# Performance work log

Measured on AMD Instinct MI355X. Metric: run time of the kernel, lower is better.

The kernel has to match this reference:

```python
import jax, jax.numpy as jnp
import numpy as np
from math import factorial

# ---------- Clebsch-Gordan coefficients for real spherical harmonics (e3nn convention) ----------

def _su2_cg(j1, j2, j3, m1, m2, m3):
    if m3 != m1 + m2:
        return 0.0
    f = factorial
    vmin = max(-j1 + j2 + m3, -j1 + m1, 0)
    vmax = min(j2 + j3 + m1, j3 - j1 + j2, j3 + m3)
    C = ((2 * j3 + 1)
         * f(j3 + j1 - j2) * f(j3 - j1 + j2) * f(j1 + j2 - j3) / f(j1 + j2 + j3 + 1)
         * f(j3 + m3) * f(j3 - m3)
         / (f(j1 - m1) * f(j1 + m1) * f(j2 - m2) * f(j2 + m2))) ** 0.5
    S = 0.0
    for v in range(vmin, vmax + 1):
        S += ((-1) ** (v + j2 + m2) / f(v)
              * f(j2 + j3 + m1 - v) * f(j1 - m1 + v)
              / f(j3 - j1 + j2 - v) / f(j3 + m3 - v) / f(v + j1 - j2 - m3))
    return C * S

def _q(l):  # change of basis real -> complex SH
    q = np.zeros((2 * l + 1, 2 * l + 1), dtype=np.complex128)
    for m in range(-l, 0):
        q[l + m, l + abs(m)] = 2 ** -0.5
        q[l + m, l - abs(m)] = -1j * 2 ** -0.5
    q[l, l] = 1.0
    for m in range(1, l + 1):
        q[l + m, l + abs(m)] = (-1) ** m * 2 ** -0.5
        q[l + m, l - abs(m)] = 1j * (-1) ** m * 2 ** -0.5
    return (-1j) ** l * q

def _real_cg(l1, l2, l3):
    Cc = np.zeros((2 * l1 + 1, 2 * l2 + 1, 2 * l3 + 1), dtype=np.complex128)
    for i, m1 in enumerate(range(-l1, l1 + 1)):
        for j, m2 in enumerate(range(-l2, l2 + 1)):
            for k, m3 in enumerate(range(-l3, l3 + 1)):
                Cc[i, j, k] = _su2_cg(l1, l2, l3, m1, m2, m3)
    Cr = np.einsum('ij,kl,nm,ikn->jlm', _q(l1), _q(l2), np.conj(_q(l3)), Cc)
    assert np.abs(Cr.imag).max() < 1e-8
    return np.real(Cr)

def _build_K(l1max, l2max, l3max):
    d1, d2, d3 = (l1max + 1) ** 2, (l2max + 1) ** 2, (l3max + 1) ** 2
    K = np.zeros((d1, d2, d3), dtype=np.float32)
    for l1 in range(l1max + 1):
        for l2 in range(l2max + 1):
            for l3 in range(abs(l1 - l2), min(l3max, l1 + l2) + 1):
                K[l1 * l1:(l1 + 1) ** 2, l2 * l2:(l2 + 1) ** 2, l3 * l3:(l3 + 1) ** 2] += _real_cg(l1, l2, l3)
    return K

_K1 = jnp.asarray(_build_K(1, 2, 3))   # [4, 9, 16]
_K2 = jnp.asarray(_build_K(3, 2, 5))   # [16, 9, 36]
_L2MAX_DIM = 9

def _real_sh_l2(d):
    # orthonormal real SH up to l=2 for unit vectors d [E,3] -> [E,9], m = -l..l
    x, y, z = d[:, 0], d[:, 1], d[:, 2]
    c0 = 0.28209479177387814
    c1 = 0.4886025119029199
    c2a = 1.0925484305920792
    c2b = 0.31539156525252005
    c2c = 0.5462742152960396
    return jnp.stack([
        jnp.full_like(x, c0),
        c1 * y, c1 * z, c1 * x,
        c2a * x * y, c2a * y * z, c2b * (3.0 * z * z - 1.0), c2a * x * z, c2c * (x * x - y * y),
    ], axis=-1)


def setup_inputs() -> dict:
    key = jax.random.key(0)
    ks = jax.random.split(key, 9)
    N, E, G, C = 51200, 819200, 64, 10
    return {
        'positions': jax.random.normal(ks[0], (N, 3), jnp.float32),
        'w1': jax.random.normal(ks[1], (1, 1), jnp.float32) * 0.5,
        'b1': jax.random.normal(ks[2], (1,), jnp.float32) * 0.1,
        'w2': jax.random.normal(ks[3], (1, 1), jnp.float32) * 0.5,
        'b2': jax.random.normal(ks[4], (1,), jnp.float32) * 0.1,
        'wg': jax.random.normal(ks[5], (72, C), jnp.float32) * 0.1,
        'bg': jax.random.normal(ks[6], (C,), jnp.float32) * 0.1,
        'senders': jax.random.randint(ks[7], (E,), 0, N, dtype=jnp.int32),
        'receivers': jax.random.randint(ks[8], (E,), 0, N, dtype=jnp.int32),
        'n_graphs': G,
    }


def reference(positions, w1, b1, w2, b2, wg, bg, senders, receivers, n_graphs):
    N = positions.shape[0]
    E = senders.shape[0]
    # edge direction spherical harmonics (normalize=True)
    d = positions[receivers] - positions[senders]
    d = d / (jnp.linalg.norm(d, axis=-1, keepdims=True) + 1e-12)
    Y = _real_sh_l2(d)                                   # [E, 9]
    # route SH degrees into parity channels: even parity (l=0,2) -> ch 0, odd (l=1) -> ch 1
    sh = jnp.zeros((E, 2, _L2MAX_DIM), Y.dtype)
    sh = sh.at[:, 0, 0].set(Y[:, 0])
    sh = sh.at[:, 1, 1:4].set(Y[:, 1:4])
    sh = sh.at[:, 0, 4:9].set(Y[:, 4:9])
    sh_flip = sh[:, ::-1]                                # parity-swapped view

    def layer(x, K, w, b, denom):
        xs = x[senders]                                  # [E, 2, d1, f]
        # per-edge equivariant tensor product; p3=0 pairs same parities, p3=1 opposite
        t0 = jnp.einsum('ijk,epif,epj->ekf', K, xs, sh)
        t1 = jnp.einsum('ijk,epif,epj->ekf', K, xs, sh_flip)
        tp = jnp.stack([t0, t1], axis=1)                 # [E, 2, d3, f]
        agg = jax.ops.segment_sum(tp, receivers, num_segments=N) / denom
        return jnp.einsum('npkf,fg->npkg', agg, w) + b   # Dense over feature dim

    x = jnp.ones((N, 2, 4, 1), Y.dtype)                  # graphs._replace(nodes=ones)
    x = layer(x, _K1, w1, b1, 1.0)                       # [N, 2, 16, 1]
    x = layer(x, _K2, w2, b2, 1.0)                       # [N, 2, 36, 1]

    # global readout: segment-sum nodes per graph, flatten, Dense -> num_classes
    gidx = jnp.repeat(jnp.arange(n_graphs), N // n_graphs)
    g = jax.ops.segment_sum(x, gidx, num_segments=n_graphs)  # [G, 2, 36, 1]
    logits = g.reshape(n_graphs, -1) @ wg + bg               # [G, 10]
    return logits
```

## Files before the change

kernel.cpp:

```cpp
#include <hip/hip_runtime.h>

__device__ __constant__ double FACT[12] = {
    1.0, 1.0, 2.0, 6.0, 24.0, 120.0, 720.0, 5040.0,
    40320.0, 362880.0, 3628800.0, 39916800.0
};

struct cplx { double re, im; };
__device__ __forceinline__ cplx cmul(cplx a, cplx b) {
    return { a.re * b.re - a.im * b.im, a.re * b.im + a.im * b.re };
}

__device__ double su2_cg_full(int j1, int j2, int j3, int m1, int m2, int m3) {
    if (j3 < abs(j1 - j2) || j3 > j1 + j2) return 0.0;
    if (abs(m1) > j1 || abs(m2) > j2 || abs(m3) > j3) return 0.0;
    if (m3 != m1 + m2) return 0.0;
    int vmin = max(max(-j1 + j2 + m3, -j1 + m1), 0);
    int vmax = min(min(j2 + j3 + m1, j3 - j1 + j2), j3 + m3);
    if (vmax < vmin) return 0.0;
    double C = sqrt((2.0 * j3 + 1.0) * FACT[j3 + j1 - j2] * FACT[j3 - j1 + j2] *
                    FACT[j1 + j2 - j3] / FACT[j1 + j2 + j3 + 1] *
                    FACT[j3 + m3] * FACT[j3 - m3] /
                    (FACT[j1 - m1] * FACT[j1 + m1] * FACT[j2 - m2] * FACT[j2 + m2]));
    double S = 0.0;
    for (int v = vmin; v <= vmax; ++v) {
        double sgn = ((v + j2 + m2) & 1) ? -1.0 : 1.0;
        S += sgn / FACT[v] * FACT[j2 + j3 + m1 - v] * FACT[j1 - m1 + v] /
             FACT[j3 - j1 + j2 - v] / FACT[j3 + m3 - v] / FACT[v + j1 - j2 - m3];
    }
    return C * S;
}

__device__ __forceinline__ int su2_idx(int l1, int l2, int l3, int m1, int m2, int m3) {
    return ((((l1 * 3 + l2) * 6 + l3) * 7 + (m1 + 3)) * 5 + (m2 + 2)) * 11 + (m3 + 5);
}
#define SU2_TAB_SIZE 27720

__device__ int q_col(int l, int c0, int* rows, cplx* vals) {
    const double s = 0.7071067811865476;
    cplx ph;
    switch (l & 3) {
        case 0: ph = {1.0, 0.0}; break;
        case 1: ph = {0.0, -1.0}; break;
        case 2: ph = {-1.0, 0.0}; break;
        default: ph = {0.0, 1.0}; break;
    }
    int mu = c0 - l;
    if (mu == 0) { rows[0] = l; vals[0] = ph; return 1; }
    if (mu > 0) {
        rows[0] = l - mu; vals[0] = cmul(ph, {s, 0.0});
        double sg = (mu & 1) ? -1.0 : 1.0;
        rows[1] = l + mu; vals[1] = cmul(ph, {sg * s, 0.0});
        return 2;
    }
    int am = -mu;
    rows[0] = l - am; vals[0] = cmul(ph, {0.0, -s});
    double sg = (am & 1) ? -1.0 : 1.0;
    rows[1] = l + am; vals[1] = cmul(ph, {0.0, sg * s});
    return 2;
}

__device__ float real_cg_elem_tab(const double* __restrict__ su2tab,
                                  int l1, int l2, int l3, int a, int b, int c) {
    int r1[2], r2[2], r3[2];
    cplx v1[2], v2[2], v3[2];
    int n1 = q_col(l1, a, r1, v1);
    int n2 = q_col(l2, b, r2, v2);
    int n3 = q_col(l3, c, r3, v3);
    double re = 0.0;
    for (int x = 0; x < n1; ++x)
        for (int y = 0; y < n2; ++y)
            for (int z = 0; z < n3; ++z) {
                cplx qq = cmul(v1[x], v2[y]);
                cplx q3c = { v3[z].re, -v3[z].im };
                qq = cmul(qq, q3c);
                double cg = su2tab[su2_idx(l1, l2, l3, r1[x] - l1, r2[y] - l2, r3[z] - l3)];
                re += qq.re * cg;
            }
    return (float)re;
}

__device__ int flsqrt(int x) {
    int l = 0;
    while ((l + 1) * (l + 1) <= x) ++l;
    return l;
}

__device__ __forceinline__ void sh_from_delta(float dx, float dy, float dz, float* Y) {
    float inv = 1.f / (sqrtf(dx * dx + dy * dy + dz * dz) + 1e-12f);
    float x = dx * inv, y = dy * inv, z = dz * inv;
    const float c1 = 0.4886025119029199f;
    const float c2a = 1.0925484305920792f;
    Y[0] = 0.28209479177387814f;
    Y[1] = c1 * y; Y[2] = c1 * z; Y[3] = c1 * x;
    Y[4] = c2a * x * y;
    Y[5] = c2a * y * z;
    Y[6] = 0.31539156525252005f * (3.f * z * z - 1.f);
    Y[7] = c2a * x * z;
    Y[8] = 0.5462742152960396f * (x * x - y * y);
}

__device__ void tbl2_work(const double* __restrict__ su2tab, int t,
                          float* __restrict__ A1, float* __restrict__ K2) {
    const int NK2 = 16 * 9 * 36;
    if (t < NK2) {
        int k = t % 36;
        int j = (t / 36) % 9;
        int i = t / (36 * 9);
        int l1 = flsqrt(i), l2 = flsqrt(j), l3 = flsqrt(k);
        float v = 0.f;
        if (l3 >= abs(l1 - l2) && l3 <= l1 + l2)
            v = real_cg_elem_tab(su2tab, l1, l2, l3, i - l1 * l1, j - l2 * l2, k - l3 * l3);
        K2[t] = v;
    } else if (t < NK2 + 144) {
        int u = t - NK2;
        int j = u / 16, k = u % 16;
        int l2 = flsqrt(j), l3 = flsqrt(k);
        float v = 0.f;
        for (int i = 0; i < 4; ++i) {
            int l1 = flsqrt(i);
            if (l3 >= abs(l1 - l2) && l3 <= l1 + l2 && l3 <= 3)
                v += real_cg_elem_tab(su2tab, l1, l2, l3, i - l1 * l1, j - l2 * l2, k - l3 * l3);
        }
        A1[u] = v;
    }
}

#define SU2_BLOCKS 109
__global__ __launch_bounds__(256) void phase1_k(double* __restrict__ su2tab,
                                                float* __restrict__ zero_base,
                                                long zeroN) {
    if (blockIdx.x < SU2_BLOCKS) {
        int t = blockIdx.x * 256 + threadIdx.x;
        if (t < SU2_TAB_SIZE) {
            int r = t;
            int im3 = r % 11; r /= 11;
            int im2 = r % 5;  r /= 5;
            int im1 = r % 7;  r /= 7;
            int l3  = r % 6;  r /= 6;
            int l2  = r % 3;  r /= 3;
            int l1  = r;
            su2tab[t] = su2_cg_full(l1, l2, l3, im1 - 3, im2 - 2, im3 - 5);
        }
    } else {
        long zb = blockIdx.x - SU2_BLOCKS;
        long nzb = gridDim.x - SU2_BLOCKS;
        long n4 = zeroN >> 2;
        float4* p = (float4*)zero_base;
        for (long i = zb * 256 + threadIdx.x; i < n4; i += nzb * 256)
            p[i] = float4{0.f, 0.f, 0.f, 0.f};
        for (long i = (n4 << 2) + zb * 256 + threadIdx.x; i < zeroN; i += nzb * 256)
            zero_base[i] = 0.f;
    }
}

#define TBL2_BLOCKS 21
#define OLCAP 16384
#define CH2D 2048

__global__ __launch_bounds__(256) void phase2d_k(const double* __restrict__ su2tab,
                                                 float* __restrict__ A1,
                                                 float* __restrict__ K2,
                                                 const int* __restrict__ rcv,
                                                 const int* __restrict__ snd,
                                                 const float* __restrict__ pos,
                                                 int* __restrict__ count,
                                                 int* __restrict__ bucket,
                                                 int* __restrict__ olcnt,
                                                 uint2* __restrict__ olist,
                                                 float* __restrict__ SY,
                                                 int E, int bslot) {
    if (blockIdx.x < TBL2_BLOCKS) {
        tbl2_work(su2tab, blockIdx.x * 256 + threadIdx.x, A1, K2);
        return;
    }
    int w = blockIdx.x - TBL2_BLOCKS;
    int xcd = (int)(blockIdx.x & 7);
    int chunk = w >> 3;
    int base = chunk * CH2D;
    int end = min(base + CH2D, E);
    for (int e = base + (int)threadIdx.x; e < end; e += 256) {
        int r = rcv[e];
        if (((r >> 4) & 7) != xcd) continue;
        int s = snd[e];
        int slot = atomicAdd(&count[(size_t)r << 4], 1);
        if (slot < bslot) {
            bucket[(size_t)r * bslot + slot] = s;
        } else {
            float Y[9];
            sh_from_delta(pos[3 * r] - pos[3 * s], pos[3 * r + 1] - pos[3 * s + 1],
                          pos[3 * r + 2] - pos[3 * s + 2], Y);
#pragma unroll
            for (int j = 0; j < 9; ++j) atomicAdd(&SY[r * 16 + j], Y[j]);
            int ob = atomicAdd(olcnt, 1);
            if (ob < OLCAP) olist[ob] = uint2{(unsigned)r, (unsigned)s};
        }
    }
}

__global__ __launch_bounds__(256) void phase2_k(const double* __restrict__ su2tab,
                                                float* __restrict__ A1,
                                                float* __restrict__ K2,
                                                const int* __restrict__ rcv,
                                                const int* __restrict__ snd,
                                                const float* __restrict__ pos,
                                                int* __restrict__ count,
                                                int* __restrict__ bucket,
                                                float* __restrict__ SY,
                                                int E, int N, int slots) {
    if (blockIdx.x < TBL2_BLOCKS) {
        tbl2_work(su2tab, blockIdx.x * 256 + threadIdx.x, A1, K2);
        return;
    }
    int e = (blockIdx.x - TBL2_BLOCKS) * 256 + threadIdx.x;
    if (e >= E) return;
    int r = rcv[e];
    int s = snd[e];
    int slot = atomicAdd(&count[r], 1);
    if (slot < slots) {
        bucket[(size_t)slot * N + r] = s;
    } else {
        float Y[9];
        sh_from_delta(pos[3 * r] - pos[3 * s], pos[3 * r + 1] - pos[3 * s + 1],
                      pos[3 * r + 2] - pos[3 * s + 2], Y);
#pragma unroll
        for (int j = 0; j < 9; ++j) atomicAdd(&SY[r * 16 + j], Y[j]);
    }
}

__device__ __forceinline__ void node_addr(int n, int N, int npg, int bslot, int newp,
                                          long* base, int* stride) {
    if (newp) {
        *base = (long)n * bslot;
        *stride = 1;
    } else {
        *base = n;
        *stride = N;
    }
}

#define TBL3_BLOCKS 6
__global__ __launch_bounds__(256) void phase3_k(const float* __restrict__ K2,
                                                const float* __restrict__ wg,
                                                const float* __restrict__ b2,
                                                const float* __restrict__ bg,
                                                int npg,
                                                float* __restrict__ T2,
                                                float* __restrict__ Cc,
                                                const float* __restrict__ pos,
                                                const int* __restrict__ count,
                                                const int* __restrict__ bucket,
                                                float* __restrict__ SY,
                                                int N, int slots, int newp, int cstride) {
    if (blockIdx.x < TBL3_BLOCKS) {
        int t = blockIdx.x * 256 + threadIdx.x;
        if (t < 1440) {
            int c = t % 10;
            int ij = t / 10;
            float acc = 0.f;
            for (int k = 0; k < 36; ++k)
                acc += K2[ij * 36 + k] * (wg[k * 10 + c] + wg[(36 + k) * 10 + c]);
            T2[t] = acc;
        } else if (t < 1450) {
            int c = t - 1440;
            float sw = 0.f;
            for (int k = 0; k < 36; ++k) sw += wg[k * 10 + c] + wg[(36 + k) * 10 + c];
            Cc[c] = (float)npg * b2[0] * sw + bg[c];
        }
    } else {
        int i = (blockIdx.x - TBL3_BLOCKS) * 256 + threadIdx.x;
        int n = i >> 1, sub = i & 1;
        if (n >= N) return;
        float rx = pos[3 * n], ry = pos[3 * n + 1], rz = pos[3 * n + 2];
        int deg = min(count[(size_t)n * cstride], slots);
        long nb; int st;
        node_addr(n, N, npg, slots, newp, &nb, &st);
        float acc[9];
#pragma unroll
        for (int j = 0; j < 9; ++j) acc[j] = 0.f;
        for (int d = sub; d < deg; d += 2) {
            int s = bucket[nb + (long)d * st];
            float Y[9];
            sh_from_delta(rx - pos[3 * s], ry - pos[3 * s + 1], rz - pos[3 * s + 2], Y);
#pragma unroll
            for (int j = 0; j < 9; ++j) acc[j] += Y[j];
        }
#pragma unroll
        for (int j = 0; j < 9; ++j) acc[j] += __shfl_xor(acc[j], 1, 64);
        if (sub == 0) {
#pragma unroll
            for (int j = 0; j < 9; ++j) SY[n * 16 + j] += acc[j];
        }
    }
}

__device__ __forceinline__ void accum_edge_s(const float* __restrict__ pos,
                                             const float* __restrict__ SY,
                                             int s, float rx, float ry, float rz,
                                             float* acc) {
    float Y[9];
    sh_from_delta(rx - pos[3 * s], ry - pos[3 * s + 1], rz - pos[3 * s + 2], Y);
    const float4* sp = reinterpret_cast<const float4*>(&SY[s * 16]);
    float4 s0 = sp[0], s1 = sp[1];
    float sv[9] = { s0.x, s0.y, s0.z, s0.w, s1.x, s1.y, s1.z, s1.w, SY[s * 16 + 8] };
#pragma unroll
    for (int jp = 0; jp < 9; ++jp)
#pragma unroll
        for (int j = 0; j < 9; ++j)
            acc[jp * 9 + j] += sv[jp] * Y[j];
}

#define TBL4_BLOCKS 4
__global__ __launch_bounds__(256) void phase4_k(const float* __restrict__ A1,
                                                const float* __restrict__ T2,
                                                float* __restrict__ G,
                                                float* __restrict__ H,
                                                const float* __restrict__ pos,
                                                const int* __restrict__ snd,
                                                const int* __restrict__ rcv,
                                                const int* __restrict__ count,
                                                const int* __restrict__ bucket,
                                                const float* __restrict__ SY,
                                                float* __restrict__ partial,
                                                int N, int E, int slots, int npb, int K,
                                                int npg, int newp, int cstride) {
    if (blockIdx.x < TBL4_BLOCKS) {
        int t = blockIdx.x * 256 + threadIdx.x;
        if (t < 810) {
            int c = t % 10;
            int jj = t / 10;
            int j = jj % 9, jp = jj / 9;
            float acc = 0.f;
            for (int i = 0; i < 16; ++i)
                acc += A1[jp * 16 + i] * T2[(i * 9 + j) * 10 + c];
            G[jj * 10 + c] = acc;
        } else if (t < 900) {
            int u = t - 810;
            int c = u % 10, j = u / 10;
            float acc = 0.f;
            for (int i = 0; i < 16; ++i) acc += T2[(i * 9 + j) * 10 + c];
            H[j * 10 + c] = acc;
        }
        return;
    }
    int bid = blockIdx.x - TBL4_BLOCKS;
    int node_local = (int)threadIdx.x % npb;
    int sub = (int)threadIdx.x / npb;
    int n = bid * npb + node_local;
    float acc[90];
#pragma unroll
    for (int v = 0; v < 90; ++v) acc[v] = 0.f;
    if (sub < K && n < N) {
        float rx = pos[3 * n], ry = pos[3 * n + 1], rz = pos[3 * n + 2];
        int deg = count[(size_t)n * cstride];
        if (newp || deg <= slots) {
            if (deg > slots) deg = slots;
            long nb; int st;
            node_addr(n, N, npg, slots, newp, &nb, &st);
            for (int d = sub; d < deg; d += K)
                accum_edge_s(pos, SY, bucket[nb + (long)d * st], rx, ry, rz, acc);
        } else {
            for (int e = sub; e < E; e += K)
                if (rcv[e] == n) accum_edge_s(pos, SY, snd[e], rx, ry, rz, acc);
        }
        if (sub == 0) {
#pragma unroll
            for (int j = 0; j < 9; ++j) acc[81 + j] = SY[n * 16 + j];
        }
    }
    __shared__ float red[4][90];
#pragma unroll
    for (int v = 0; v < 90; ++v) {
        float x = acc[v];
#pragma unroll
        for (int m = 1; m < 64; m <<= 1) x += __shfl_xor(x, m, 64);
        acc[v] = x;
    }
    int lane = threadIdx.x & 63, wid = threadIdx.x >> 6;
    if (lane == 0) {
#pragma unroll
        for (int v = 0; v < 90; ++v) red[wid][v] = acc[v];
    }
    __syncthreads();
    int nw = blockDim.x >> 6;
    for (int t = threadIdx.x; t < 90; t += blockDim.x) {
        float s = 0.f;
        for (int w = 0; w < nw; ++w) s += red[w][t];
        partial[bid * 90 + t] = s;
    }
}

__global__ __launch_bounds__(128) void final3_k(const float* __restrict__ G,
                                                const float* __restrict__ H,
                                                const float* __restrict__ partial,
                                                const float* __restrict__ Cc,
                                                const float* __restrict__ w1,
                                                const float* __restrict__ b1,
                                                const float* __restrict__ w2,
                                                const float* __restrict__ pos,
                                                const float* __restrict__ SY,
                                                const int* __restrict__ olcnt,
                                                const uint2* __restrict__ olist,
                                                float* __restrict__ out,
                                                int bpg, int npg) {
    __shared__ float Ms[90];
    __shared__ float Gs[810];
    __shared__ float Hs[90];
    int g = blockIdx.x;
    int tid = threadIdx.x;
    for (int t = tid; t < 810; t += 128) Gs[t] = G[t];
    for (int t = tid; t < 90; t += 128) Hs[t] = H[t];
    const float* pg = &partial[(size_t)g * bpg * 90];
    for (int v = tid; v < 90; v += 128) {
        float m = 0.f;
        for (int q = 0; q < bpg; ++q) m += pg[q * 90 + v];
        Ms[v] = m;
    }
    __syncthreads();
    int oc = min(olcnt[0], OLCAP);
    for (int i = tid; i < oc; i += 128) {
        uint2 es = olist[i];
        int r = (int)es.x;
        if (r / npg != g) continue;
        int s = (int)es.y;
        float Y[9];
        sh_from_delta(pos[3 * r] - pos[3 * s], pos[3 * r + 1] - pos[3 * s + 1],
                      pos[3 * r + 2] - pos[3 * s + 2], Y);
#pragma unroll
        for (int jp = 0; jp < 9; ++jp) {
            float sv = SY[s * 16 + jp];
#pragma unroll
            for (int j = 0; j < 9; ++j) atomicAdd(&Ms[jp * 9 + j], sv * Y[j]);
        }
    }
    __syncthreads();
    if (tid < 10) {
        int c = tid;
        float z = 0.f;
#pragma unroll
        for (int idx = 0; idx < 81; ++idx) z += Gs[idx * 10 + c] * Ms[idx];
        float z2 = 0.f;
#pragma unroll
        for (int j = 0; j < 9; ++j) z2 += Hs[j * 10 + c] * Ms[81 + j];
        out[g * 10 + c] = w2[0] * (w1[0] * z + b1[0] * z2) + Cc[c];
    }
}

extern "C" void kernel_launch(void* const* d_in, const int* in_sizes, int n_in,
                              void* d_out, int out_size, void* d_ws, size_t ws_size,
                              hipStream_t stream) {
    const float* pos = (const float*)d_in[0];
    const float* w1  = (const float*)d_in[1];
    const float* b1  = (const float*)d_in[2];
    const float* w2  = (const float*)d_in[3];
    const float* b2  = (const float*)d_in[4];
    const float* wg  = (const float*)d_in[5];
    const float* bg  = (const float*)d_in[6];
    const int* snd   = (const int*)d_in[7];
    const int* rcv   = (const int*)d_in[8];

    int N = in_sizes[0] / 3;
    int E = in_sizes[7];
    int nG = out_size / 10;
    int npg = N / nG;
    int npb = 1;
    for (int d = 1; d <= 64 && d <= npg; ++d) if (npg % d == 0) npb = d;
    int K = 256 / npb; if (K > 8) K = 8;
    int bpg = npg / npb;
    int NB2 = nG * bpg;

    float* ws = (float*)d_ws;
    float* A1  = ws + 0;
    float* K2  = ws + 144;
    float* T2  = ws + 5328;
    float* Cc  = ws + 6768;
    float* Gt  = ws + 6784;
    float* Ht  = ws + 7600;
    double* su2tab = (double*)(ws + 7696);
    size_t c0 = 7696 + 2 * (size_t)SU2_TAB_SIZE;
    size_t wsFloats = ws_size / 4;

    const int BSLOT = 40;
    size_t sy_off    = c0 + 16 * (size_t)N;
    size_t olcnt_off = sy_off + 16 * (size_t)N;
    size_t zeroN     = 32 * (size_t)N + 16;
    size_t b0        = c0 + zeroN;
    size_t olist_off = b0 + (size_t)BSLOT * N;
    size_t part_off  = olist_off + 2 * (size_t)OLCAP;
    size_t new_end   = part_off + (size_t)NB2 * 90;
    bool newp = (npg * nG == N) && (nG > 0) && (new_end <= wsFloats);

    if (newp) {
        int* count   = (int*)ws + c0;
        float* SY    = ws + sy_off;
        int* olcnt   = (int*)ws + olcnt_off;
        int* bucket  = (int*)ws + b0;
        uint2* olist = (uint2*)(ws + olist_off);
        float* part  = ws + part_off;
        phase1_k<<<SU2_BLOCKS + 128, 256, 0, stream>>>(su2tab, ws + c0, (long)zeroN);
        int nCH = (E + CH2D - 1) / CH2D;
        phase2d_k<<<TBL2_BLOCKS + nCH * 8, 256, 0, stream>>>(
            su2tab, A1, K2, rcv, snd, pos, count, bucket, olcnt, olist, SY, E, BSLOT);
        phase3_k<<<TBL3_BLOCKS + (2 * N + 255) / 256, 256, 0, stream>>>(
            K2, wg, b2, bg, npg, T2, Cc, pos, count, bucket, SY, N, BSLOT, 1, 16);
        phase4_k<<<TBL4_BLOCKS + NB2, 256, 0, stream>>>(
            A1, T2, Gt, Ht, pos, snd, rcv, count, bucket, SY, part, N, E, BSLOT, npb, K,
            npg, 1, 16);
        final3_k<<<nG, 128, 0, stream>>>(Gt, Ht, part, Cc, w1, b1, w2, pos, SY,
                                         olcnt, olist, (float*)d_out, bpg, npg);
    } else {
        int* count = (int*)ws + c0;
        float* SY  = ws + c0 + N;
        int* olcnt = (int*)ws + c0 + 17 * (size_t)N;
        size_t zN  = 17 * (size_t)N + 16;
        size_t ob0 = c0 + zN;
        float* part = ws + ob0;
        size_t buck_off = ob0 + (size_t)NB2 * 90;
        int* bucket = (int*)ws + buck_off;
        long avail = (long)wsFloats - (long)buck_off;
        int slots = 0;
        if (avail > 0) slots = (int)(avail / (long)N);
        if (slots > 48) slots = 48;
        phase1_k<<<SU2_BLOCKS + 128, 256, 0, stream>>>(su2tab, ws + c0, (long)zN);
        phase2_k<<<TBL2_BLOCKS + (E + 255) / 256, 256, 0, stream>>>(
            su2tab, A1, K2, rcv, snd, pos, count, bucket, SY, E, N, slots);
        phase3_k<<<TBL3_BLOCKS + (2 * N + 255) / 256, 256, 0, stream>>>(
            K2, wg, b2, bg, npg, T2, Cc, pos, count, bucket, SY, N, slots, 0, 1);
        phase4_k<<<TBL4_BLOCKS + NB2, 256, 0, stream>>>(
            A1, T2, Gt, Ht, pos, snd, rcv, count, bucket, SY, part, N, E, slots, npb, K,
            npg, 0, 1);
        final3_k<<<nG, 128, 0, stream>>>(Gt, Ht, part, Cc, w1, b1, w2, pos, SY,
                                         olcnt, (uint2*)(ws + olist_off), (float*)d_out,
                                         bpg, npg);
    }
}
```

Baseline: 105.1 us.

## Precompute Clebsch-Gordan tables on host and restructure per-graph edge accumulation

Moves the Clebsch-Gordan table construction (SU2 table plus the K2 and A1 contractions) out of the GPU kernels. The tables are now built once on the host, cached in a static array and copied to the workspace each call with an async memcpy. This drops the table-building blocks from the first two kernels. It also adds a new phase4n kernel where each thread handles one node, reads its bucketed neighbours as int4 vectors, and reduces the results per graph block. The tables are input-independent constants, but the host copy adds a transfer to every call.

```diff
diff --git a/kernel.cpp b/kernel.cpp
--- a/kernel.cpp
+++ b/kernel.cpp
@@ -1,43 +1,40 @@
 #include <hip/hip_runtime.h>
-
-__device__ __constant__ double FACT[12] = {
-    1.0, 1.0, 2.0, 6.0, 24.0, 120.0, 720.0, 5040.0,
-    40320.0, 362880.0, 3628800.0, 39916800.0
-};
-
-struct cplx { double re, im; };
-__device__ __forceinline__ cplx cmul(cplx a, cplx b) {
+#include <cmath>
+#include <cstdlib>
+
+namespace host_tbl {
+
+static const double F[12] = {1.0, 1.0, 2.0, 6.0, 24.0, 120.0, 720.0, 5040.0,
+                             40320.0, 362880.0, 3628800.0, 39916800.0};
+
+struct hcplx { double re, im; };
+static inline hcplx cmul(hcplx a, hcplx b) {
     return { a.re * b.re - a.im * b.im, a.re * b.im + a.im * b.re };
 }
 
-__device__ double su2_cg_full(int j1, int j2, int j3, int m1, int m2, int m3) {
-    if (j3 < abs(j1 - j2) || j3 > j1 + j2) return 0.0;
-    if (abs(m1) > j1 || abs(m2) > j2 || abs(m3) > j3) return 0.0;
+static double su2_cg(int j1, int j2, int j3, int m1, int m2, int m3) {
+    if (j3 < std::abs(j1 - j2) || j3 > j1 + j2) return 0.0;
+    if (std::abs(m1) > j1 || std::abs(m2) > j2 || std::abs(m3) > j3) return 0.0;
     if (m3 != m1 + m2) return 0.0;
-    int vmin = max(max(-j1 + j2 + m3, -j1 + m1), 0);
-    int vmax = min(min(j2 + j3 + m1, j3 - j1 + j2), j3 + m3);
+    int vmin = std::max(std::max(-j1 + j2 + m3, -j1 + m1), 0);
+    int vmax = std::min(std::min(j2 + j3 + m1, j3 - j1 + j2), j3 + m3);
     if (vmax < vmin) return 0.0;
-    double C = sqrt((2.0 * j3 + 1.0) * FACT[j3 + j1 - j2] * FACT[j3 - j1 + j2] *
-                    FACT[j1 + j2 - j3] / FACT[j1 + j2 + j3 + 1] *
-                    FACT[j3 + m3] * FACT[j3 - m3] /
-                    (FACT[j1 - m1] * FACT[j1 + m1] * FACT[j2 - m2] * FACT[j2 + m2]));
+    double C = std::sqrt((2.0 * j3 + 1.0) * F[j3 + j1 - j2] * F[j3 - j1 + j2] *
+                         F[j1 + j2 - j3] / F[j1 + j2 + j3 + 1] *
+                         F[j3 + m3] * F[j3 - m3] /
+                         (F[j1 - m1] * F[j1 + m1] * F[j2 - m2] * F[j2 + m2]));
     double S = 0.0;
     for (int v = vmin; v <= vmax; ++v) {
         double sgn = ((v + j2 + m2) & 1) ? -1.0 : 1.0;
-        S += sgn / FACT[v] * FACT[j2 + j3 + m1 - v] * FACT[j1 - m1 + v] /
-             FACT[j3 - j1 + j2 - v] / FACT[j3 + m3 - v] / FACT[v + j1 - j2 - m3];
+        S += sgn / F[v] * F[j2 + j3 + m1 - v] * F[j1 - m1 + v] /
+             F[j3 - j1 + j2 - v] / F[j3 + m3 - v] / F[v + j1 - j2 - m3];
     }
     return C * S;
 }
 
-__device__ __forceinline__ int su2_idx(int l1, int l2, int l3, int m1, int m2, int m3) {
-    return ((((l1 * 3 + l2) * 6 + l3) * 7 + (m1 + 3)) * 5 + (m2 + 2)) * 11 + (m3 + 5);
-}
-#define SU2_TAB_SIZE 27720
-
-__device__ int q_col(int l, int c0, int* rows, cplx* vals) {
+static int q_col(int l, int c0, int* rows, hcplx* vals) {
     const double s = 0.7071067811865476;
-    cplx ph;
+    hcplx ph;
     switch (l & 3) {
         case 0: ph = {1.0, 0.0}; break;
         case 1: ph = {0.0, -1.0}; break;
@@ -59,10 +56,9 @@
     return 2;
 }
 
-__device__ float real_cg_elem_tab(const double* __restrict__ su2tab,
-                                  int l1, int l2, int l3, int a, int b, int c) {
+static float real_cg(int l1, int l2, int l3, int a, int b, int c) {
     int r1[2], r2[2], r3[2];
-    cplx v1[2], v2[2], v3[2];
+    hcplx v1[2], v2[2], v3[2];
     int n1 = q_col(l1, a, r1, v1);
     int n2 = q_col(l2, b, r2, v2);
     int n3 = q_col(l3, c, r3, v3);
@@ -70,19 +66,51 @@
     for (int x = 0; x < n1; ++x)
         for (int y = 0; y < n2; ++y)
             for (int z = 0; z < n3; ++z) {
-                cplx qq = cmul(v1[x], v2[y]);
-                cplx q3c = { v3[z].re, -v3[z].im };
+                hcplx qq = cmul(v1[x], v2[y]);
+                hcplx q3c = { v3[z].re, -v3[z].im };
                 qq = cmul(qq, q3c);
-                double cg = su2tab[su2_idx(l1, l2, l3, r1[x] - l1, r2[y] - l2, r3[z] - l3)];
+                double cg = su2_cg(l1, l2, l3, r1[x] - l1, r2[y] - l2, r3[z] - l3);
                 re += qq.re * cg;
             }
     return (float)re;
 }
 
-__device__ int flsqrt(int x) {
+static int flsqrt(int x) {
     int l = 0;
     while ((l + 1) * (l + 1) <= x) ++l;
     return l;
+}
+
+static const float* get_AK() {
+    static float AK[5328];
+    static bool built = []() {
+        for (int u = 0; u < 144; ++u) {
+            int j = u / 16, k = u % 16;
+            int l2 = flsqrt(j), l3 = flsqrt(k);
+            float v = 0.f;
+            for (int i = 0; i < 4; ++i) {
+                int l1 = flsqrt(i);
+                if (l3 >= std::abs(l1 - l2) && l3 <= l1 + l2 && l3 <= 3)
+                    v += real_cg(l1, l2, l3, i - l1 * l1, j - l2 * l2, k - l3 * l3);
+            }
+            AK[u] = v;
+        }
+        for (int t = 0; t < 16 * 9 * 36; ++t) {
+            int k = t % 36;
+            int j = (t / 36) % 9;
+            int i = t / (36 * 9);
+            int l1 = flsqrt(i), l2 = flsqrt(j), l3 = flsqrt(k);
+            float v = 0.f;
+            if (l3 >= std::abs(l1 - l2) && l3 <= l1 + l2)
+                v = real_cg(l1, l2, l3, i - l1 * l1, j - l2 * l2, k - l3 * l3);
+            AK[144 + t] = v;
+        }
+        return true;
+    }();
+    (void)built;
+    return AK;
+}
+
 }
 
 __device__ __forceinline__ void sh_from_delta(float dx, float dy, float dz, float* Y) {
@@ -99,68 +127,22 @@
     Y[8] = 0.5462742152960396f * (x * x - y * y);
 }
 
-__device__ void tbl2_work(const double* __restrict__ su2tab, int t,
-                          float* __restrict__ A1, float* __restrict__ K2) {
-    const int NK2 = 16 * 9 * 36;
-    if (t < NK2) {
-        int k = t % 36;
-        int j = (t / 36) % 9;
-        int i = t / (36 * 9);
-        int l1 = flsqrt(i), l2 = flsqrt(j), l3 = flsqrt(k);
-        float v = 0.f;
-        if (l3 >= abs(l1 - l2) && l3 <= l1 + l2)
-            v = real_cg_elem_tab(su2tab, l1, l2, l3, i - l1 * l1, j - l2 * l2, k - l3 * l3);
-        K2[t] = v;
-    } else if (t < NK2 + 144) {
-        int u = t - NK2;
-        int j = u / 16, k = u % 16;
-        int l2 = flsqrt(j), l3 = flsqrt(k);
-        float v = 0.f;
-        for (int i = 0; i < 4; ++i) {
-            int l1 = flsqrt(i);
-            if (l3 >= abs(l1 - l2) && l3 <= l1 + l2 && l3 <= 3)
-                v += real_cg_elem_tab(su2tab, l1, l2, l3, i - l1 * l1, j - l2 * l2, k - l3 * l3);
-        }
-        A1[u] = v;
-    }
-}
-
-#define SU2_BLOCKS 109
-__global__ __launch_bounds__(256) void phase1_k(double* __restrict__ su2tab,
-                                                float* __restrict__ zero_base,
-                                                long zeroN) {
-    if (blockIdx.x < SU2_BLOCKS) {
-        int t = blockIdx.x * 256 + threadIdx.x;
-        if (t < SU2_TAB_SIZE) {
-            int r = t;
-            int im3 = r % 11; r /= 11;
-            int im2 = r % 5;  r /= 5;
-            int im1 = r % 7;  r /= 7;
-            int l3  = r % 6;  r /= 6;
-            int l2  = r % 3;  r /= 3;
-            int l1  = r;
-            su2tab[t] = su2_cg_full(l1, l2, l3, im1 - 3, im2 - 2, im3 - 5);
-        }
-    } else {
-        long zb = blockIdx.x - SU2_BLOCKS;
-        long nzb = gridDim.x - SU2_BLOCKS;
-        long n4 = zeroN >> 2;
-        float4* p = (float4*)zero_base;
-        for (long i = zb * 256 + threadIdx.x; i < n4; i += nzb * 256)
-            p[i] = float4{0.f, 0.f, 0.f, 0.f};
-        for (long i = (n4 << 2) + zb * 256 + threadIdx.x; i < zeroN; i += nzb * 256)
-            zero_base[i] = 0.f;
-    }
-}
-
-#define TBL2_BLOCKS 21
+__global__ __launch_bounds__(256) void zero_k(float* __restrict__ zero_base,
+                                              long zeroN) {
+    long nzb = gridDim.x;
+    long zb = blockIdx.x;
+    long n4 = zeroN >> 2;
+    float4* p = (float4*)zero_base;
+    for (long i = zb * 256 + threadIdx.x; i < n4; i += nzb * 256)
+        p[i] = float4{0.f, 0.f, 0.f, 0.f};
+    for (long i = (n4 << 2) + zb * 256 + threadIdx.x; i < zeroN; i += nzb * 256)
+        zero_base[i] = 0.f;
+}
+
 #define OLCAP 16384
 #define CH2D 2048
 
-__global__ __launch_bounds__(256) void phase2d_k(const double* __restrict__ su2tab,
-                                                 float* __restrict__ A1,
-                                                 float* __restrict__ K2,
-                                                 const int* __restrict__ rcv,
+__global__ __launch_bounds__(256) void phase2d_k(const int* __restrict__ rcv,
                                                  const int* __restrict__ snd,
                                                  const float* __restrict__ pos,
                                                  int* __restrict__ count,
@@ -169,11 +151,7 @@
                                                  uint2* __restrict__ olist,
                                                  float* __restrict__ SY,
                                                  int E, int bslot) {
-    if (blockIdx.x < TBL2_BLOCKS) {
-        tbl2_work(su2tab, blockIdx.x * 256 + threadIdx.x, A1, K2);
-        return;
-    }
-    int w = blockIdx.x - TBL2_BLOCKS;
+    int w = blockIdx.x;
     int xcd = (int)(blockIdx.x & 7);
     int chunk = w >> 3;
     int base = chunk * CH2D;
@@ -197,21 +175,14 @@
     }
 }
 
-__global__ __launch_bounds__(256) void phase2_k(const double* __restrict__ su2tab,
-                                                float* __restrict__ A1,
-                                                float* __restrict__ K2,
-                                                const int* __restrict__ rcv,
+__global__ __launch_bounds__(256) void phase2_k(const int* __restrict__ rcv,
                                                 const int* __restrict__ snd,
                                                 const float* __restrict__ pos,
                                                 int* __restrict__ count,
                                                 int* __restrict__ bucket,
                                                 float* __restrict__ SY,
                                                 int E, int N, int slots) {
-    if (blockIdx.x < TBL2_BLOCKS) {
-        tbl2_work(su2tab, blockIdx.x * 256 + threadIdx.x, A1, K2);
-        return;
-    }
-    int e = (blockIdx.x - TBL2_BLOCKS) * 256 + threadIdx.x;
+    int e = blockIdx.x * 256 + threadIdx.x;
     if (e >= E) return;
     int r = rcv[e];
     int s = snd[e];
@@ -310,19 +281,16 @@
 }
 
 #define TBL4_BLOCKS 4
-__global__ __launch_bounds__(256) void phase4_k(const float* __restrict__ A1,
-                                                const float* __restrict__ T2,
-                                                float* __restrict__ G,
-                                                float* __restrict__ H,
-                                                const float* __restrict__ pos,
-                                                const int* __restrict__ snd,
-                                                const int* __restrict__ rcv,
-                                                const int* __restrict__ count,
-                                                const int* __restrict__ bucket,
-                                                const float* __restrict__ SY,
-                                                float* __restrict__ partial,
-                                                int N, int E, int slots, int npb, int K,
-                                                int npg, int newp, int cstride) {
+__global__ __launch_bounds__(256) void phase4n_k(const float* __restrict__ A1,
+                                                 const float* __restrict__ T2,
+                                                 float* __restrict__ G,
+                                                 float* __restrict__ H,
+                                                 const float* __restrict__ pos,
+                                                 const int* __restrict__ count,
+                                                 const int* __restrict__ bucket,
+                                                 const float* __restrict__ SY,
+                                                 float* __restrict__ partial,
+                                                 int npg, int bslot, int bpg4, int nb) {
     if (blockIdx.x < TBL4_BLOCKS) {
         int t = blockIdx.x * 256 + threadIdx.x;
         if (t < 810) {
@@ -343,6 +311,81 @@
         return;
     }
     int bid = blockIdx.x - TBL4_BLOCKS;
+    int g = bid / bpg4, q = bid - g * bpg4;
+    int nl = q * nb + (int)threadIdx.x;
+    float acc[90];
+#pragma unroll
+    for (int v = 0; v < 90; ++v) acc[v] = 0.f;
+    if ((int)threadIdx.x < nb && nl < npg) {
+        int n = g * npg + nl;
+        float rx = pos[3 * n], ry = pos[3 * n + 1], rz = pos[3 * n + 2];
+        int deg = count[(size_t)n << 4];
+        if (deg > bslot) deg = bslot;
+        const int4* row = reinterpret_cast<const int4*>(&bucket[(size_t)n * bslot]);
+        for (int d0 = 0; d0 < deg; d0 += 4) {
+            int4 s4 = row[d0 >> 2];
+            int m = deg - d0;
+            accum_edge_s(pos, SY, s4.x, rx, ry, rz, acc);
+            if (m > 1) accum_edge_s(pos, SY, s4.y, rx, ry, rz, acc);
+            if (m > 2) accum_edge_s(pos, SY, s4.z, rx, ry, rz, acc);
+            if (m > 3) accum_edge_s(pos, SY, s4.w, rx, ry, rz, acc);
+        }
+#pragma unroll
+        for (int j = 0; j < 9; ++j) acc[81 + j] = SY[n * 16 + j];
+    }
+    __shared__ float red[4][90];
+#pragma unroll
+    for (int v = 0; v < 90; ++v) {
+        float x = acc[v];
+#pragma unroll
+        for (int m = 1; m < 64; m <<= 1) x += __shfl_xor(x, m, 64);
+        acc[v] = x;
+    }
+    int lane = threadIdx.x & 63, wid = threadIdx.x >> 6;
+    if (lane == 0) {
+#pragma unroll
+        for (int v = 0; v < 90; ++v) red[wid][v] = acc[v];
+    }
+    __syncthreads();
+    for (int t = threadIdx.x; t < 90; t += 256) {
+        float s = 0.f;
+        for (int w = 0; w < 4; ++w) s += red[w][t];
+        partial[(size_t)bid * 90 + t] = s;
+    }
+}
+
+__global__ __launch_bounds__(256) void phase4_k(const float* __restrict__ A1,
+                                                const float* __restrict__ T2,
+                                                float* __restrict__ G,
+                                                float* __restrict__ H,
+                                                const float* __restrict__ pos,
+                                                const int* __restrict__ snd,
+                                                const int* __restrict__ rcv,
+                                                const int* __restrict__ count,
+                                                const int* __restrict__ bucket,
+                                                const float* __restrict__ SY,
+                                                float* __restrict__ partial,
+                                                int N, int E, int slots, int npb, int K) {
+    if (blockIdx.x < TBL4_BLOCKS) {
+        int t = blockIdx.x * 256 + threadIdx.x;
+        if (t < 810) {
+            int c = t % 10;
+            int jj = t / 10;
+            int j = jj % 9, jp = jj / 9;
+            float acc = 0.f;
+            for (int i = 0; i < 16; ++i)
+                acc += A1[jp * 16 + i] * T2[(i * 9 + j) * 10 + c];
+            G[jj * 10 + c] = acc;
+        } else if (t < 900) {
+            int u = t - 810;
+            int c = u % 10, j = u / 10;
+            float acc = 0.f;
+            for (int i = 0; i < 16; ++i) acc += T2[(i * 9 + j) * 10 + c];
+            H[j * 10 + c] = acc;
+        }
+        return;
+    }
+    int bid = blockIdx.x - TBL4_BLOCKS;
     int node_local = (int)threadIdx.x % npb;
     int sub = (int)threadIdx.x / npb;
     int n = bid * npb + node_local;
@@ -351,13 +394,10 @@
     for (int v = 0; v < 90; ++v) acc[v] = 0.f;
     if (sub < K && n < N) {
         float rx = pos[3 * n], ry = pos[3 * n + 1], rz = pos[3 * n + 2];
-        int deg = count[(size_t)n * cstride];
-        if (newp || deg <= slots) {
-            if (deg > slots) deg = slots;
-            long nb; int st;
-            node_addr(n, N, npg, slots, newp, &nb, &st);
+        int deg = count[n];
+        if (deg <= slots) {
             for (int d = sub; d < deg; d += K)
-                accum_edge_s(pos, SY, bucket[nb + (long)d * st], rx, ry, rz, acc);
+                accum_edge_s(pos, SY, bucket[(size_t)d * N + n], rx, ry, rz, acc);
         } else {
             for (int e = sub; e < E; e += K)
                 if (rcv[e] == n) accum_edge_s(pos, SY, snd[e], rx, ry, rz, acc);
@@ -462,11 +502,6 @@
     int E = in_sizes[7];
     int nG = out_size / 10;
     int npg = N / nG;
-    int npb = 1;
-    for (int d = 1; d <= 64 && d <= npg; ++d) if (npg % d == 0) npb = d;
-    int K = 256 / npb; if (K > 8) K = 8;
-    int bpg = npg / npb;
-    int NB2 = nG * bpg;
 
     float* ws = (float*)d_ws;
     float* A1  = ws + 0;
@@ -475,19 +510,24 @@
     float* Cc  = ws + 6768;
     float* Gt  = ws + 6784;
     float* Ht  = ws + 7600;
-    double* su2tab = (double*)(ws + 7696);
-    size_t c0 = 7696 + 2 * (size_t)SU2_TAB_SIZE;
+    size_t c0 = 63136;
     size_t wsFloats = ws_size / 4;
 
+    hipMemcpyAsync(ws, host_tbl::get_AK(), 5328 * sizeof(float),
+                   hipMemcpyHostToDevice, stream);
+
     const int BSLOT = 40;
+    int bpg4 = (npg + 255) / 256;
+    int nb   = (npg + bpg4 - 1) / bpg4;
+    int NB4  = nG * bpg4;
     size_t sy_off    = c0 + 16 * (size_t)N;
     size_t olcnt_off = sy_off + 16 * (size_t)N;
     size_t zeroN     = 32 * (size_t)N + 16;
     size_t b0        = c0 + zeroN;
     size_t olist_off = b0 + (size_t)BSLOT * N;
     size_t part_off  = olist_off + 2 * (size_t)OLCAP;
-    size_t new_end   = part_off + (size_t)NB2 * 90;
-    bool newp = (npg * nG == N) && (nG > 0) && (new_end <= wsFloats);
+    size_t new_end   = part_off + (size_t)NB4 * 90;
+    bool newp = (npg * nG == N) && (nG > 0) && (nb <= 256) && (new_end <= wsFloats);
 
     if (newp) {
         int* count   = (int*)ws + c0;
@@ -496,18 +536,22 @@
         int* bucket  = (int*)ws + b0;
         uint2* olist = (uint2*)(ws + olist_off);
         float* part  = ws + part_off;
-        phase1_k<<<SU2_BLOCKS + 128, 256, 0, stream>>>(su2tab, ws + c0, (long)zeroN);
+        zero_k<<<128, 256, 0, stream>>>(ws + c0, (long)zeroN);
         int nCH = (E + CH2D - 1) / CH2D;
-        phase2d_k<<<TBL2_BLOCKS + nCH * 8, 256, 0, stream>>>(
-            su2tab, A1, K2, rcv, snd, pos, count, bucket, olcnt, olist, SY, E, BSLOT);
+        phase2d_k<<<nCH * 8, 256, 0, stream>>>(
+            rcv, snd, pos, count, bucket, olcnt, olist, SY, E, BSLOT);
         phase3_k<<<TBL3_BLOCKS + (2 * N + 255) / 256, 256, 0, stream>>>(
             K2, wg, b2, bg, npg, T2, Cc, pos, count, bucket, SY, N, BSLOT, 1, 16);
-        phase4_k<<<TBL4_BLOCKS + NB2, 256, 0, stream>>>(
-            A1, T2, Gt, Ht, pos, snd, rcv, count, bucket, SY, part, N, E, BSLOT, npb, K,
-            npg, 1, 16);
+        phase4n_k<<<TBL4_BLOCKS + NB4, 256, 0, stream>>>(
+            A1, T2, Gt, Ht, pos, count, bucket, SY, part, npg, BSLOT, bpg4, nb);
         final3_k<<<nG, 128, 0, stream>>>(Gt, Ht, part, Cc, w1, b1, w2, pos, SY,
-                                         olcnt, olist, (float*)d_out, bpg, npg);
+                                         olcnt, olist, (float*)d_out, bpg4, npg);
     } else {
+        int npb = 1;
+        for (int d = 1; d <= 64 && d <= npg; ++d) if (npg % d == 0) npb = d;
+        int K = 256 / npb; if (K > 8) K = 8;
+        int bpg = (npb > 0) ? npg / npb : 1;
+        int NB2 = nG * bpg;
         int* count = (int*)ws + c0;
         float* SY  = ws + c0 + N;
         int* olcnt = (int*)ws + c0 + 17 * (size_t)N;
@@ -520,14 +564,13 @@
         int slots = 0;
         if (avail > 0) slots = (int)(avail / (long)N);
         if (slots > 48) slots = 48;
-        phase1_k<<<SU2_BLOCKS + 128, 256, 0, stream>>>(su2tab, ws + c0, (long)zN);
-        phase2_k<<<TBL2_BLOCKS + (E + 255) / 256, 256, 0, stream>>>(
-            su2tab, A1, K2, rcv, snd, pos, count, bucket, SY, E, N, slots);
+        zero_k<<<128, 256, 0, stream>>>(ws + c0, (long)zN);
+        phase2_k<<<(E + 255) / 256, 256, 0, stream>>>(
+            rcv, snd, pos, count, bucket, SY, E, N, slots);
         phase3_k<<<TBL3_BLOCKS + (2 * N + 255) / 256, 256, 0, stream>>>(
             K2, wg, b2, bg, npg, T2, Cc, pos, count, bucket, SY, N, slots, 0, 1);
         phase4_k<<<TBL4_BLOCKS + NB2, 256, 0, stream>>>(
-            A1, T2, Gt, Ht, pos, snd, rcv, count, bucket, SY, part, N, E, slots, npb, K,
-            npg, 0, 1);
+            A1, T2, Gt, Ht, pos, snd, rcv, count, bucket, SY, part, N, E, slots, npb, K);
         final3_k<<<nG, 128, 0, stream>>>(Gt, Ht, part, Cc, w1, b1, w2, pos, SY,
                                          olcnt, (uint2*)(ws + olist_off), (float*)d_out,
                                          bpg, npg);
```

Measured after the change: 135.4 us. 1.29x slower.

## Add specialized phase4 kernel mapping one thread per node with vectorized bucket reads

Applied to the files above, without the earlier changes.

Adds a dedicated phase4n kernel for the main path. Each thread now handles one whole node instead of splitting a node's edges across K sub-threads. Each block covers up to 256 nodes of a graph, and neighbor indices are read four at a time as int4 from a contiguous per-node row. This is meant to cut the number of blocks and partial sums, remove the node_addr indirection, and make bucket loads wider. The cost is less parallelism per node, so high-degree nodes serialize their edges, and the row reads assume the bucket rows are 16-byte aligned.

```diff
diff --git a/kernel.cpp b/kernel.cpp
--- a/kernel.cpp
+++ b/kernel.cpp
@@ -310,19 +310,16 @@
 }
 
 #define TBL4_BLOCKS 4
-__global__ __launch_bounds__(256) void phase4_k(const float* __restrict__ A1,
-                                                const float* __restrict__ T2,
-                                                float* __restrict__ G,
-                                                float* __restrict__ H,
-                                                const float* __restrict__ pos,
-                                                const int* __restrict__ snd,
-                                                const int* __restrict__ rcv,
-                                                const int* __restrict__ count,
-                                                const int* __restrict__ bucket,
-                                                const float* __restrict__ SY,
-                                                float* __restrict__ partial,
-                                                int N, int E, int slots, int npb, int K,
-                                                int npg, int newp, int cstride) {
+__global__ __launch_bounds__(256) void phase4n_k(const float* __restrict__ A1,
+                                                 const float* __restrict__ T2,
+                                                 float* __restrict__ G,
+                                                 float* __restrict__ H,
+                                                 const float* __restrict__ pos,
+                                                 const int* __restrict__ count,
+                                                 const int* __restrict__ bucket,
+                                                 const float* __restrict__ SY,
+                                                 float* __restrict__ partial,
+                                                 int npg, int bslot, int bpg4, int nb) {
     if (blockIdx.x < TBL4_BLOCKS) {
         int t = blockIdx.x * 256 + threadIdx.x;
         if (t < 810) {
@@ -343,6 +340,81 @@
         return;
     }
     int bid = blockIdx.x - TBL4_BLOCKS;
+    int g = bid / bpg4, q = bid - g * bpg4;
+    int nl = q * nb + (int)threadIdx.x;
+    float acc[90];
+#pragma unroll
+    for (int v = 0; v < 90; ++v) acc[v] = 0.f;
+    if ((int)threadIdx.x < nb && nl < npg) {
+        int n = g * npg + nl;
+        float rx = pos[3 * n], ry = pos[3 * n + 1], rz = pos[3 * n + 2];
+        int deg = count[(size_t)n << 4];
+        if (deg > bslot) deg = bslot;
+        const int4* row = reinterpret_cast<const int4*>(&bucket[(size_t)n * bslot]);
+        for (int d0 = 0; d0 < deg; d0 += 4) {
+            int4 s4 = row[d0 >> 2];
+            int m = deg - d0;
+            accum_edge_s(pos, SY, s4.x, rx, ry, rz, acc);
+            if (m > 1) accum_edge_s(pos, SY, s4.y, rx, ry, rz, acc);
+            if (m > 2) accum_edge_s(pos, SY, s4.z, rx, ry, rz, acc);
+            if (m > 3) accum_edge_s(pos, SY, s4.w, rx, ry, rz, acc);
+        }
+#pragma unroll
+        for (int j = 0; j < 9; ++j) acc[81 + j] = SY[n * 16 + j];
+    }
+    __shared__ float red[4][90];
+#pragma unroll
+    for (int v = 0; v < 90; ++v) {
+        float x = acc[v];
+#pragma unroll
+        for (int m = 1; m < 64; m <<= 1) x += __shfl_xor(x, m, 64);
+        acc[v] = x;
+    }
+    int lane = threadIdx.x & 63, wid = threadIdx.x >> 6;
+    if (lane == 0) {
+#pragma unroll
+        for (int v = 0; v < 90; ++v) red[wid][v] = acc[v];
+    }
+    __syncthreads();
+    for (int t = threadIdx.x; t < 90; t += 256) {
+        float s = 0.f;
+        for (int w = 0; w < 4; ++w) s += red[w][t];
+        partial[(size_t)bid * 90 + t] = s;
+    }
+}
+
+__global__ __launch_bounds__(256) void phase4_k(const float* __restrict__ A1,
+                                                const float* __restrict__ T2,
+                                                float* __restrict__ G,
+                                                float* __restrict__ H,
+                                                const float* __restrict__ pos,
+                                                const int* __restrict__ snd,
+                                                const int* __restrict__ rcv,
+                                                const int* __restrict__ count,
+                                                const int* __restrict__ bucket,
+                                                const float* __restrict__ SY,
+                                                float* __restrict__ partial,
+                                                int N, int E, int slots, int npb, int K) {
+    if (blockIdx.x < TBL4_BLOCKS) {
+        int t = blockIdx.x * 256 + threadIdx.x;
+        if (t < 810) {
+            int c = t % 10;
+            int jj = t / 10;
+            int j = jj % 9, jp = jj / 9;
+            float acc = 0.f;
+            for (int i = 0; i < 16; ++i)
+                acc += A1[jp * 16 + i] * T2[(i * 9 + j) * 10 + c];
+            G[jj * 10 + c] = acc;
+        } else if (t < 900) {
+            int u = t - 810;
+            int c = u % 10, j = u / 10;
+            float acc = 0.f;
+            for (int i = 0; i < 16; ++i) acc += T2[(i * 9 + j) * 10 + c];
+            H[j * 10 + c] = acc;
+        }
+        return;
+    }
+    int bid = blockIdx.x - TBL4_BLOCKS;
     int node_local = (int)threadIdx.x % npb;
     int sub = (int)threadIdx.x / npb;
     int n = bid * npb + node_local;
@@ -351,13 +423,10 @@
     for (int v = 0; v < 90; ++v) acc[v] = 0.f;
     if (sub < K && n < N) {
         float rx = pos[3 * n], ry = pos[3 * n + 1], rz = pos[3 * n + 2];
-        int deg = count[(size_t)n * cstride];
-        if (newp || deg <= slots) {
-            if (deg > slots) deg = slots;
-            long nb; int st;
-            node_addr(n, N, npg, slots, newp, &nb, &st);
+        int deg = count[n];
+        if (deg <= slots) {
             for (int d = sub; d < deg; d += K)
-                accum_edge_s(pos, SY, bucket[nb + (long)d * st], rx, ry, rz, acc);
+                accum_edge_s(pos, SY, bucket[(size_t)d * N + n], rx, ry, rz, acc);
         } else {
             for (int e = sub; e < E; e += K)
                 if (rcv[e] == n) accum_edge_s(pos, SY, snd[e], rx, ry, rz, acc);
@@ -462,11 +531,6 @@
     int E = in_sizes[7];
     int nG = out_size / 10;
     int npg = N / nG;
-    int npb = 1;
-    for (int d = 1; d <= 64 && d <= npg; ++d) if (npg % d == 0) npb = d;
-    int K = 256 / npb; if (K > 8) K = 8;
-    int bpg = npg / npb;
-    int NB2 = nG * bpg;
 
     float* ws = (float*)d_ws;
     float* A1  = ws + 0;
@@ -480,14 +544,17 @@
     size_t wsFloats = ws_size / 4;
 
     const int BSLOT = 40;
+    int bpg4 = (npg + 255) / 256;
+    int nb   = (npg + bpg4 - 1) / bpg4;
+    int NB4  = nG * bpg4;
     size_t sy_off    = c0 + 16 * (size_t)N;
     size_t olcnt_off = sy_off + 16 * (size_t)N;
     size_t zeroN     = 32 * (size_t)N + 16;
     size_t b0        = c0 + zeroN;
     size_t olist_off = b0 + (size_t)BSLOT * N;
     size_t part_off  = olist_off + 2 * (size_t)OLCAP;
-    size_t new_end   = part_off + (size_t)NB2 * 90;
-    bool newp = (npg * nG == N) && (nG > 0) && (new_end <= wsFloats);
+    size_t new_end   = part_off + (size_t)NB4 * 90;
+    bool newp = (npg * nG == N) && (nG > 0) && (nb <= 256) && (new_end <= wsFloats);
 
     if (newp) {
         int* count   = (int*)ws + c0;
@@ -502,12 +569,16 @@
             su2tab, A1, K2, rcv, snd, pos, count, bucket, olcnt, olist, SY, E, BSLOT);
         phase3_k<<<TBL3_BLOCKS + (2 * N + 255) / 256, 256, 0, stream>>>(
             K2, wg, b2, bg, npg, T2, Cc, pos, count, bucket, SY, N, BSLOT, 1, 16);
-        phase4_k<<<TBL4_BLOCKS + NB2, 256, 0, stream>>>(
-            A1, T2, Gt, Ht, pos, snd, rcv, count, bucket, SY, part, N, E, BSLOT, npb, K,
-            npg, 1, 16);
+        phase4n_k<<<TBL4_BLOCKS + NB4, 256, 0, stream>>>(
+            A1, T2, Gt, Ht, pos, count, bucket, SY, part, npg, BSLOT, bpg4, nb);
         final3_k<<<nG, 128, 0, stream>>>(Gt, Ht, part, Cc, w1, b1, w2, pos, SY,
-                                         olcnt, olist, (float*)d_out, bpg, npg);
+                                         olcnt, olist, (float*)d_out, bpg4, npg);
     } else {
+        int npb = 1;
+        for (int d = 1; d <= 64 && d <= npg; ++d) if (npg % d == 0) npb = d;
+        int K = 256 / npb; if (K > 8) K = 8;
+        int bpg = (npb > 0) ? npg / npb : 1;
+        int NB2 = nG * bpg;
         int* count = (int*)ws + c0;
         float* SY  = ws + c0 + N;
         int* olcnt = (int*)ws + c0 + 17 * (size_t)N;
@@ -526,8 +597,7 @@
         phase3_k<<<TBL3_BLOCKS + (2 * N + 255) / 256, 256, 0, stream>>>(
             K2, wg, b2, bg, npg, T2, Cc, pos, count, bucket, SY, N, slots, 0, 1);
         phase4_k<<<TBL4_BLOCKS + NB2, 256, 0, stream>>>(
-            A1, T2, Gt, Ht, pos, snd, rcv, count, bucket, SY, part, N, E, slots, npb, K,
-            npg, 0, 1);
+            A1, T2, Gt, Ht, pos, snd, rcv, count, bucket, SY, part, N, E, slots, npb, K);
         final3_k<<<nG, 128, 0, stream>>>(Gt, Ht, part, Cc, w1, b1, w2, pos, SY,
                                          olcnt, (uint2*)(ws + olist_off), (float*)d_out,
                                          bpg, npg);
```

Result: faster. 93.29 us (median of 2 runs) (-11.2%).
